# Optimization experiments

Hardware: AMD Instinct MI355X
Metric: run time of the kernel (lower is better)

The kernel has to match this reference:

```python
import jax, jax.numpy as jnp
import numpy as np

B, N, D, K, S = 16, 1024, 256, 16, 512
TEMP = 0.5   # self.temperature, set externally in the repo
EPS = 1e-10


def _gumbel(key, shape):
    u = jax.random.uniform(key, shape, dtype=jnp.float32)
    return -jnp.log(-jnp.log(u + EPS) + EPS)


def setup_inputs() -> dict:
    key = jax.random.key(0)
    k1, k2, k3 = jax.random.split(key, 3)
    return {
        "ze": jax.random.normal(k1, (B, N, D), dtype=jnp.float32),
        "c_logits": jax.random.normal(k2, (B, K), dtype=jnp.float32),
        "books": jax.random.normal(k3, (K, S, D), dtype=jnp.float32),
        "log_param_q": jnp.asarray(np.log(0.5), dtype=jnp.float32),
        "log_param_q_cls": jnp.asarray(np.log(0.5), dtype=jnp.float32),
        "is_train": 1,
    }


def reference(ze, c_logits, books, log_param_q, log_param_q_cls, is_train):
    # training-path forward of GaussianVectorQuantizer
    param_q = 1.0 + jnp.exp(log_param_q)
    precision_q = 0.5 / jnp.clip(param_q, 1e-10)
    param_q_cls = 1.0 + jnp.exp(log_param_q_cls)
    precision_q_cls = 0.5 / jnp.clip(param_q_cls, 1e-10)

    gkey = jax.random.key(42)
    kg1, kg2 = jax.random.split(gkey)

    # gumbel-softmax over clusters: (B, K)
    c_probs = jax.nn.softmax(
        (c_logits * precision_q_cls + _gumbel(kg1, c_logits.shape)) / TEMP, axis=-1
    )

    # pairwise squared distances to every codebook entry of every cluster: (B, N, K, S)
    z2 = jnp.sum(ze * ze, axis=-1)[:, :, None, None]          # (B, N, 1, 1)
    b2 = jnp.sum(books * books, axis=-1)[None, None]          # (1, 1, K, S)
    cross = jnp.einsum('bnd,ksd->bnks', ze, books)            # (B, N, K, S)
    logit_all = -(z2 - 2.0 * cross + b2) * precision_q        # (B, N, K, S)

    # cluster-probability-weighted logits: (B, N, S)
    logits = jnp.einsum('bnks,bk->bns', logit_all, c_probs)

    # gumbel-softmax encodings per cluster, then weighted codebook matmul
    enc = jax.nn.softmax((logit_all + _gumbel(kg2, logit_all.shape)) / TEMP, axis=-1)
    zq = jnp.einsum('bnks,ksd,bk->bnd', enc, books, c_probs)  # (B, N, D)

    prob = jax.nn.softmax(logits, axis=-1)
    log_prob = jax.nn.log_softmax(logits, axis=-1)
    return zq, precision_q, prob, log_prob
```

## Files before the change

### kernel.cpp

```cpp
#include <hip/hip_runtime.h>
#include <cstdint>
#include <cstddef>

#define JAX_PARTITIONABLE 1

namespace {

constexpr int Bsz = 16, Nn = 1024, Dd = 256, Kk = 16, Ss = 512;
constexpr uint32_t BN = (uint32_t)Bsz * Nn;
constexpr int ZQ_SIZE = Bsz * Nn * Dd;
constexpr int PQ_OFF = ZQ_SIZE;
constexpr int PROB_OFF = ZQ_SIZE + 1;
constexpr int BNS = Bsz * Nn * Ss;
constexpr int LP_OFF = PROB_OFF + BNS;

constexpr int WS_CP = 0;
constexpr int WS_B2 = 256;
constexpr int WS_WB2 = WS_B2 + Kk * Ss;
constexpr int WS_WBOOKS = WS_WB2 + Bsz * Ss;
constexpr int WS_BBF = WS_WBOOKS + Bsz * Ss * Dd;
constexpr int WS_BTF = WS_BBF + (Kk * Ss * Dd) / 2;

typedef __attribute__((ext_vector_type(8))) short bf16x8;
typedef __attribute__((ext_vector_type(4))) short short4v;
typedef __attribute__((ext_vector_type(4))) float f32x4;

struct KP { uint32_t a, b; };

__host__ __device__ constexpr KP tf2x32(uint32_t k0, uint32_t k1,
                                        uint32_t x0, uint32_t x1) {
  uint32_t ks[3] = {k0, k1, k0 ^ k1 ^ 0x1BD11BDAu};
  const int rot[2][4] = {{13, 15, 26, 6}, {17, 29, 16, 24}};
  x0 += ks[0];
  x1 += ks[1];
#pragma unroll
  for (int i = 0; i < 5; ++i) {
#pragma unroll
    for (int j = 0; j < 4; ++j) {
      int r = rot[i & 1][j];
      x0 += x1;
      x1 = (x1 << r) | (x1 >> (32 - r));
      x1 ^= x0;
    }
    x0 += ks[(i + 1) % 3];
    x1 += ks[(i + 2) % 3] + (uint32_t)(i + 1);
  }
  return {x0, x1};
}

#if JAX_PARTITIONABLE
constexpr KP KG1 = tf2x32(0u, 42u, 0u, 0u);
constexpr KP KG2 = tf2x32(0u, 42u, 0u, 1u);
#else
constexpr KP KH0 = tf2x32(0u, 42u, 0u, 2u);
constexpr KP KH1 = tf2x32(0u, 42u, 1u, 3u);
constexpr KP KG1 = {KH0.a, KH1.a};
constexpr KP KG2 = {KH0.b, KH1.b};
#endif

__device__ __forceinline__ float jax_gumbel(KP key, uint32_t idx, uint32_t half) {
#if JAX_PARTITIONABLE
  (void)half;
  KP h = tf2x32(key.a, key.b, 0u, idx);
  uint32_t bits = h.a ^ h.b;
#else
  uint32_t lo = idx < half ? idx : idx - half;
  KP h = tf2x32(key.a, key.b, lo, lo + half);
  uint32_t bits = idx < half ? h.a : h.b;
#endif
  float u = __uint_as_float((bits >> 9) | 0x3F800000u) - 1.0f;
  return -__logf(-__logf(u + 1e-10f) + 1e-10f);
}

__device__ __forceinline__ float prec_q(const float* p) {
  return 0.5f / fmaxf(1.0f + expf(p[0]), 1e-10f);
}

__device__ __forceinline__ short f2bf(float x) {
  uint32_t u = __float_as_uint(x);
  uint32_t r = (u + 0x7FFFu + ((u >> 16) & 1u)) >> 16;
  return (short)r;
}

__global__ void __launch_bounds__(256) cprobs_kernel(
    const float* __restrict__ c_logits, const float* __restrict__ lpq,
    const float* __restrict__ lpq_cls, float* __restrict__ ws,
    float* __restrict__ out) {
  __shared__ float sl[256];
  const int t = threadIdx.x;
  const float pqc = prec_q(lpq_cls);
  float g = jax_gumbel(KG1, (uint32_t)t, 128u);
  sl[t] = (c_logits[t] * pqc + g) * 2.0f;
  __syncthreads();
  const int b = t >> 4;
  float m = -3.0e38f;
  for (int j = 0; j < 16; ++j) m = fmaxf(m, sl[b * 16 + j]);
  float sum = 0.f;
  for (int j = 0; j < 16; ++j) sum += expf(sl[b * 16 + j] - m);
  ws[WS_CP + t] = expf(sl[t] - m) / sum;
  if (t == 0) out[PQ_OFF] = prec_q(lpq);
}

__global__ void __launch_bounds__(256) norms_kernel(
    const float* __restrict__ books, float* __restrict__ ws) {
  const int row = blockIdx.x * 4 + (threadIdx.x >> 6);
  const int lane = threadIdx.x & 63;
  float4 v = ((const float4*)(books + (size_t)row * Dd))[lane];
  float s = v.x * v.x + v.y * v.y + v.z * v.z + v.w * v.w;
#pragma unroll
  for (int d = 1; d < 64; d <<= 1) s += __shfl_xor(s, d);
  if (lane == 0) ws[WS_B2 + row] = s;
}

__global__ void __launch_bounds__(256) prep_kernel(
    const float* __restrict__ books, float* __restrict__ ws) {
  __shared__ short tile[16 * 256];
  const int k = blockIdx.x >> 5;
  const int s0 = (blockIdx.x & 31) << 4;
  short* bbf = (short*)(ws + WS_BBF);
  short* btf = (short*)(ws + WS_BTF);
  const int t = threadIdx.x;
#pragma unroll
  for (int i = 0; i < 4; ++i) {
    int idx = t + 256 * i;
    int r = idx >> 6, dq = idx & 63;
    float4 v = ((const float4*)books)[(size_t)(k * Ss + s0 + r) * 64 + dq];
    short4v h = {f2bf(v.x), f2bf(v.y), f2bf(v.z), f2bf(v.w)};
    *(short4v*)&bbf[(size_t)(k * Ss + s0 + r) * 256 + dq * 4] = h;
    *(short4v*)&tile[r * 256 + dq * 4] = h;
  }
  __syncthreads();
  const int d = t;
  short vals[16];
#pragma unroll
  for (int r = 0; r < 16; ++r) vals[r] = tile[r * 256 + d];
  bf16x8 lo, hi;
#pragma unroll
  for (int r = 0; r < 8; ++r) { lo[r] = vals[r]; hi[r] = vals[r + 8]; }
  size_t base = ((size_t)(k * 256 + d)) * 512 + s0;
  *(bf16x8*)&btf[base] = lo;
  *(bf16x8*)&btf[base + 8] = hi;
}

__global__ void __launch_bounds__(256) wbooks_kernel(
    const float* __restrict__ books, float* __restrict__ ws) {
  const int bs = blockIdx.x;
  const int b = bs >> 9, s = bs & 511;
  const int d = threadIdx.x;
  const float* cp = ws + WS_CP + b * 16;
  float acc = 0.f;
#pragma unroll
  for (int k = 0; k < 16; ++k)
    acc = fmaf(cp[k], books[((size_t)(k * Ss + s)) * Dd + d], acc);
  ws[WS_WBOOKS + ((size_t)(b * Ss + s)) * Dd + d] = acc;
  if (d == 0) {
    float a2 = 0.f;
#pragma unroll
    for (int k = 0; k < 16; ++k) a2 = fmaf(cp[k], ws[WS_B2 + k * Ss + s], a2);
    ws[WS_WB2 + b * Ss + s] = a2;
  }
}

__global__ void __launch_bounds__(256, 4) logits_kernel(
    const float* __restrict__ ze, const float* __restrict__ lpq,
    const float* __restrict__ ws, float* __restrict__ out) {
  __shared__ float ze_s[8 * 256];
  __shared__ float ls[8 * 512];
  const int b = blockIdx.x >> 7;
  const int n0 = (blockIdx.x & 127) << 3;
  const int t = threadIdx.x;
  const float pq = prec_q(lpq);

  {
    const float4* zin = (const float4*)(ze + (size_t)(b * Nn + n0) * Dd);
    float4* zo = (float4*)ze_s;
    zo[t] = zin[t];
    zo[t + 256] = zin[t + 256];
  }
  __syncthreads();

  float acc0[8], acc1[8];
#pragma unroll
  for (int r = 0; r < 8; ++r) { acc0[r] = 0.f; acc1[r] = 0.f; }
  const int s0 = t, s1 = t + 256;
  const float4* w4_0 = (const float4*)(ws + WS_WBOOKS + (size_t)(b * Ss + s0) * Dd);
  const float4* w4_1 = (const float4*)(ws + WS_WBOOKS + (size_t)(b * Ss + s1) * Dd);
  const float4* z4 = (const float4*)ze_s;
  for (int dq = 0; dq < 64; ++dq) {
    float4 u0 = w4_0[dq], u1 = w4_1[dq];
#pragma unroll
    for (int r = 0; r < 8; ++r) {
      float4 z = z4[r * 64 + dq];
      acc0[r] = fmaf(z.x, u0.x, fmaf(z.y, u0.y, fmaf(z.z, u0.z, fmaf(z.w, u0.w, acc0[r]))));
      acc1[r] = fmaf(z.x, u1.x, fmaf(z.y, u1.y, fmaf(z.z, u1.z, fmaf(z.w, u1.w, acc1[r]))));
    }
  }
  const float wb2v0 = ws[WS_WB2 + b * Ss + s0];
  const float wb2v1 = ws[WS_WB2 + b * Ss + s1];
#pragma unroll
  for (int r = 0; r < 8; ++r) {
    ls[r * 512 + s0] = pq * (2.f * acc0[r] - wb2v0);
    ls[r * 512 + s1] = pq * (2.f * acc1[r] - wb2v1);
  }
  __syncthreads();

  const int r = t >> 5, c = t & 31;
  float m = -3.0e38f;
#pragma unroll
  for (int j = 0; j < 16; ++j) m = fmaxf(m, ls[r * 512 + c + 32 * j]);
#pragma unroll
  for (int d = 1; d < 32; d <<= 1) m = fmaxf(m, __shfl_xor(m, d));
  float ev[16];
  float sum = 0.f;
#pragma unroll
  for (int j = 0; j < 16; ++j) {
    ev[j] = expf(ls[r * 512 + c + 32 * j] - m);
    sum += ev[j];
  }
#pragma unroll
  for (int d = 1; d < 32; d <<= 1) sum += __shfl_xor(sum, d);
  const float inv = 1.f / sum;
  const float lsum = logf(sum);
  const size_t obase = (size_t)(b * Nn + n0 + r) * Ss;
  float* pr = out + PROB_OFF + obase;
  float* lp = out + LP_OFF + obase;
#pragma unroll
  for (int j = 0; j < 16; ++j) {
    int s = c + 32 * j;
    pr[s] = ev[j] * inv;
    lp[s] = (ls[r * 512 + s] - m) - lsum;
  }
}

__global__ void __launch_bounds__(512, 4) zq_kernel(
    const float* __restrict__ ze, const float* __restrict__ lpq,
    const float* __restrict__ ws, float* __restrict__ out) {
  __shared__ short ze_s[32 * 264];
  __shared__ short enc_s[32 * 520];
  __shared__ float redmax[8][32];
  __shared__ float redsum[8][32];
  __shared__ float finalM[32];
  __shared__ float finalT[32];
  __shared__ float cpk[16];

  const int b = blockIdx.x >> 5;
  const int n0 = (blockIdx.x & 31) << 5;
  const int t = threadIdx.x;
  const int w = t >> 6, lane = t & 63, c = lane & 15, q = lane >> 4;
  const float pq = prec_q(lpq);
  const short* bbf = (const short*)(ws + WS_BBF);
  const short* btf = (const short*)(ws + WS_BTF);
  const float* b2p = ws + WS_B2;

  if (t < 16) cpk[t] = ws[WS_CP + b * 16 + t];
#pragma unroll
  for (int i = 0; i < 4; ++i) {
    int idx = t + 512 * i;
    int r = idx >> 6, dq = idx & 63;
    float4 v = ((const float4*)ze)[(size_t)(b * Nn + n0 + r) * 64 + dq];
    short4v h = {f2bf(v.x), f2bf(v.y), f2bf(v.z), f2bf(v.w)};
    *(short4v*)&ze_s[r * 264 + dq * 4] = h;
  }
  __syncthreads();

  f32x4 acc2[2][2];
#pragma unroll
  for (int rt = 0; rt < 2; ++rt)
#pragma unroll
    for (int dt = 0; dt < 2; ++dt) acc2[rt][dt] = (f32x4)(0.f);

  for (int k = 0; k < 16; ++k) {
    f32x4 acc1[2][4];
#pragma unroll
    for (int rt = 0; rt < 2; ++rt)
#pragma unroll
      for (int st = 0; st < 4; ++st) acc1[rt][st] = (f32x4)(0.f);
    for (int dstep = 0; dstep < 8; ++dstep) {
      bf16x8 a0 = *(const bf16x8*)&ze_s[(c) * 264 + dstep * 32 + q * 8];
      bf16x8 a1 = *(const bf16x8*)&ze_s[(16 + c) * 264 + dstep * 32 + q * 8];
#pragma unroll
      for (int st = 0; st < 4; ++st) {
        bf16x8 bB = *(const bf16x8*)&bbf[((size_t)(k * Ss + w * 64 + st * 16 + c)) * 256 +
                                         dstep * 32 + q * 8];
        acc1[0][st] = __builtin_amdgcn_mfma_f32_16x16x32_bf16(a0, bB, acc1[0][st], 0, 0, 0);
        acc1[1][st] = __builtin_amdgcn_mfma_f32_16x16x32_bf16(a1, bB, acc1[1][st], 0, 0, 0);
      }
    }

    float b2v[4];
#pragma unroll
    for (int st = 0; st < 4; ++st) b2v[st] = b2p[k * Ss + w * 64 + st * 16 + c];
    float mx[2][4], sm[2][4];
#pragma unroll
    for (int rt = 0; rt < 2; ++rt)
#pragma unroll
      for (int reg = 0; reg < 4; ++reg) mx[rt][reg] = -3.0e38f;
#pragma unroll
    for (int rt = 0; rt < 2; ++rt)
#pragma unroll
      for (int st = 0; st < 4; ++st)
#pragma unroll
        for (int reg = 0; reg < 4; ++reg) {
          int row = n0 + rt * 16 + q * 4 + reg;
          uint32_t gi = ((uint32_t)(b * Nn + row) * (uint32_t)Kk + (uint32_t)k) * (uint32_t)Ss +
                        (uint32_t)(w * 64 + st * 16 + c);
          float g = jax_gumbel(KG2, gi, 0u);
          float v = ((2.f * acc1[rt][st][reg] - b2v[st]) * pq + g) * 2.f;
          acc1[rt][st][reg] = v;
          mx[rt][reg] = fmaxf(mx[rt][reg], v);
        }
#pragma unroll
    for (int m = 1; m < 16; m <<= 1)
#pragma unroll
      for (int rt = 0; rt < 2; ++rt)
#pragma unroll
        for (int reg = 0; reg < 4; ++reg)
          mx[rt][reg] = fmaxf(mx[rt][reg], __shfl_xor(mx[rt][reg], m));
#pragma unroll
    for (int rt = 0; rt < 2; ++rt)
#pragma unroll
      for (int reg = 0; reg < 4; ++reg) sm[rt][reg] = 0.f;
#pragma unroll
    for (int rt = 0; rt < 2; ++rt)
#pragma unroll
      for (int st = 0; st < 4; ++st)
#pragma unroll
        for (int reg = 0; reg < 4; ++reg) {
          float e = __expf(acc1[rt][st][reg] - mx[rt][reg]);
          acc1[rt][st][reg] = e;
          sm[rt][reg] += e;
        }
#pragma unroll
    for (int m = 1; m < 16; m <<= 1)
#pragma unroll
      for (int rt = 0; rt < 2; ++rt)
#pragma unroll
        for (int reg = 0; reg < 4; ++reg) sm[rt][reg] += __shfl_xor(sm[rt][reg], m);
    if (c == 0) {
#pragma unroll
      for (int rt = 0; rt < 2; ++rt)
#pragma unroll
        for (int reg = 0; reg < 4; ++reg) {
          int rl = rt * 16 + q * 4 + reg;
          redmax[w][rl] = mx[rt][reg];
          redsum[w][rl] = sm[rt][reg];
        }
    }
    __syncthreads();
    if (t < 32) {
      float M = redmax[0][t];
#pragma unroll
      for (int w2 = 1; w2 < 8; ++w2) M = fmaxf(M, redmax[w2][t]);
      float T = 0.f;
#pragma unroll
      for (int w2 = 0; w2 < 8; ++w2) T += redsum[w2][t] * __expf(redmax[w2][t] - M);
      finalM[t] = M;
      finalT[t] = 1.f / T;
    }
    __syncthreads();

    const float cpv = cpk[k];
#pragma unroll
    for (int rt = 0; rt < 2; ++rt)
#pragma unroll
      for (int reg = 0; reg < 4; ++reg) {
        int rl = rt * 16 + q * 4 + reg;
        float scale = cpv * __expf(mx[rt][reg] - finalM[rl]) * finalT[rl];
#pragma unroll
        for (int st = 0; st < 4; ++st)
          enc_s[rl * 520 + w * 64 + st * 16 + c] = f2bf(acc1[rt][st][reg] * scale);
      }
    __syncthreads();

    for (int ss = 0; ss < 16; ++ss) {
      bf16x8 a0 = *(const bf16x8*)&enc_s[(c) * 520 + ss * 32 + q * 8];
      bf16x8 a1 = *(const bf16x8*)&enc_s[(16 + c) * 520 + ss * 32 + q * 8];
#pragma unroll
      for (int dt = 0; dt < 2; ++dt) {
        bf16x8 bB = *(const bf16x8*)&btf[((size_t)(k * 256 + w * 32 + dt * 16 + c)) * 512 +
                                         ss * 32 + q * 8];
        acc2[0][dt] = __builtin_amdgcn_mfma_f32_16x16x32_bf16(a0, bB, acc2[0][dt], 0, 0, 0);
        acc2[1][dt] = __builtin_amdgcn_mfma_f32_16x16x32_bf16(a1, bB, acc2[1][dt], 0, 0, 0);
      }
    }
    __syncthreads();
  }

#pragma unroll
  for (int rt = 0; rt < 2; ++rt)
#pragma unroll
    for (int dt = 0; dt < 2; ++dt)
#pragma unroll
      for (int reg = 0; reg < 4; ++reg) {
        int row = n0 + rt * 16 + q * 4 + reg;
        int d = w * 32 + dt * 16 + c;
        out[(size_t)(b * Nn + row) * Dd + d] = acc2[rt][dt][reg];
      }
}

}

extern "C" void kernel_launch(void* const* d_in, const int* in_sizes, int n_in,
                              void* d_out, int out_size, void* d_ws, size_t ws_size,
                              hipStream_t stream) {
  (void)in_sizes; (void)n_in; (void)out_size; (void)ws_size;
  const float* ze = (const float*)d_in[0];
  const float* c_logits = (const float*)d_in[1];
  const float* books = (const float*)d_in[2];
  const float* lpq = (const float*)d_in[3];
  const float* lpq_cls = (const float*)d_in[4];
  float* out = (float*)d_out;
  float* ws = (float*)d_ws;

  hipLaunchKernelGGL(cprobs_kernel, dim3(1), dim3(256), 0, stream,
                     c_logits, lpq, lpq_cls, ws, out);
  hipLaunchKernelGGL(norms_kernel, dim3(Kk * Ss / 4), dim3(256), 0, stream, books, ws);
  hipLaunchKernelGGL(prep_kernel, dim3(Kk * 32), dim3(256), 0, stream, books, ws);
  hipLaunchKernelGGL(wbooks_kernel, dim3(Bsz * Ss), dim3(256), 0, stream, books, ws);
  hipLaunchKernelGGL(logits_kernel, dim3(Bsz * (Nn / 8)), dim3(256), 0, stream,
                     ze, lpq, ws, out);
  hipLaunchKernelGGL(zq_kernel, dim3(Bsz * (Nn / 32)), dim3(512), 0, stream,
                     ze, lpq, ws, out);
}
```

Before: 885.0 us.

## Shrink zq_kernel row tile to 16 with 256-thread blocks and fewer barriers

New measurement: 1.216 ms. 1.37x slower.

```diff
diff --git a/kernel.cpp b/kernel.cpp
--- a/kernel.cpp
+++ b/kernel.cpp
@@ -232,19 +232,17 @@
   }
 }
 
-__global__ void __launch_bounds__(512, 4) zq_kernel(
+__global__ void __launch_bounds__(256, 4) zq_kernel(
     const float* __restrict__ ze, const float* __restrict__ lpq,
     const float* __restrict__ ws, float* __restrict__ out) {
-  __shared__ short ze_s[32 * 264];
-  __shared__ short enc_s[32 * 520];
-  __shared__ float redmax[8][32];
-  __shared__ float redsum[8][32];
-  __shared__ float finalM[32];
-  __shared__ float finalT[32];
+  __shared__ short ze_s[16 * 264];
+  __shared__ short enc_s[16 * 520];
+  __shared__ float redmax[4][16];
+  __shared__ float redsum[4][16];
   __shared__ float cpk[16];
 
-  const int b = blockIdx.x >> 5;
-  const int n0 = (blockIdx.x & 31) << 5;
+  const int b = blockIdx.x >> 6;
+  const int n0 = (blockIdx.x & 63) << 4;
   const int t = threadIdx.x;
   const int w = t >> 6, lane = t & 63, c = lane & 15, q = lane >> 4;
   const float pq = prec_q(lpq);
@@ -255,7 +253,7 @@
   if (t < 16) cpk[t] = ws[WS_CP + b * 16 + t];
 #pragma unroll
   for (int i = 0; i < 4; ++i) {
-    int idx = t + 512 * i;
+    int idx = t + 256 * i;
     int r = idx >> 6, dq = idx & 63;
     float4 v = ((const float4*)ze)[(size_t)(b * Nn + n0 + r) * 64 + dq];
     short4v h = {f2bf(v.x), f2bf(v.y), f2bf(v.z), f2bf(v.w)};
@@ -263,139 +261,110 @@
   }
   __syncthreads();
 
-  f32x4 acc2[2][2];
-#pragma unroll
-  for (int rt = 0; rt < 2; ++rt)
-#pragma unroll
-    for (int dt = 0; dt < 2; ++dt) acc2[rt][dt] = (f32x4)(0.f);
+  f32x4 acc2[4];
+#pragma unroll
+  for (int dt = 0; dt < 4; ++dt) acc2[dt] = (f32x4)(0.f);
+
+  const uint32_t rowbase = (uint32_t)(b * Nn + n0 + q * 4);
 
   for (int k = 0; k < 16; ++k) {
-    f32x4 acc1[2][4];
-#pragma unroll
-    for (int rt = 0; rt < 2; ++rt)
-#pragma unroll
-      for (int st = 0; st < 4; ++st) acc1[rt][st] = (f32x4)(0.f);
+    f32x4 acc1[8];
+#pragma unroll
+    for (int st = 0; st < 8; ++st) acc1[st] = (f32x4)(0.f);
     for (int dstep = 0; dstep < 8; ++dstep) {
-      bf16x8 a0 = *(const bf16x8*)&ze_s[(c) * 264 + dstep * 32 + q * 8];
-      bf16x8 a1 = *(const bf16x8*)&ze_s[(16 + c) * 264 + dstep * 32 + q * 8];
-#pragma unroll
-      for (int st = 0; st < 4; ++st) {
-        bf16x8 bB = *(const bf16x8*)&bbf[((size_t)(k * Ss + w * 64 + st * 16 + c)) * 256 +
+      bf16x8 a0 = *(const bf16x8*)&ze_s[c * 264 + dstep * 32 + q * 8];
+#pragma unroll
+      for (int st = 0; st < 8; ++st) {
+        bf16x8 bB = *(const bf16x8*)&bbf[((size_t)(k * Ss + w * 128 + st * 16 + c)) * 256 +
                                          dstep * 32 + q * 8];
-        acc1[0][st] = __builtin_amdgcn_mfma_f32_16x16x32_bf16(a0, bB, acc1[0][st], 0, 0, 0);
-        acc1[1][st] = __builtin_amdgcn_mfma_f32_16x16x32_bf16(a1, bB, acc1[1][st], 0, 0, 0);
-      }
-    }
-
-    float b2v[4];
-#pragma unroll
-    for (int st = 0; st < 4; ++st) b2v[st] = b2p[k * Ss + w * 64 + st * 16 + c];
-    float mx[2][4], sm[2][4];
-#pragma unroll
-    for (int rt = 0; rt < 2; ++rt)
-#pragma unroll
-      for (int reg = 0; reg < 4; ++reg) mx[rt][reg] = -3.0e38f;
-#pragma unroll
-    for (int rt = 0; rt < 2; ++rt)
-#pragma unroll
-      for (int st = 0; st < 4; ++st)
-#pragma unroll
-        for (int reg = 0; reg < 4; ++reg) {
-          int row = n0 + rt * 16 + q * 4 + reg;
-          uint32_t gi = ((uint32_t)(b * Nn + row) * (uint32_t)Kk + (uint32_t)k) * (uint32_t)Ss +
-                        (uint32_t)(w * 64 + st * 16 + c);
-          float g = jax_gumbel(KG2, gi, 0u);
-          float v = ((2.f * acc1[rt][st][reg] - b2v[st]) * pq + g) * 2.f;
-          acc1[rt][st][reg] = v;
-          mx[rt][reg] = fmaxf(mx[rt][reg], v);
-        }
+        acc1[st] = __builtin_amdgcn_mfma_f32_16x16x32_bf16(a0, bB, acc1[st], 0, 0, 0);
+      }
+    }
+
+    float b2v[8];
+#pragma unroll
+    for (int st = 0; st < 8; ++st) b2v[st] = b2p[k * Ss + w * 128 + st * 16 + c];
+    float mx[4], sm[4];
+#pragma unroll
+    for (int reg = 0; reg < 4; ++reg) mx[reg] = -3.0e38f;
+#pragma unroll
+    for (int st = 0; st < 8; ++st)
+#pragma unroll
+      for (int reg = 0; reg < 4; ++reg) {
+        uint32_t gi = ((rowbase + reg) * (uint32_t)Kk + (uint32_t)k) * (uint32_t)Ss +
+                      (uint32_t)(w * 128 + st * 16 + c);
+        float g = jax_gumbel(KG2, gi, 0u);
+        float v = ((2.f * acc1[st][reg] - b2v[st]) * pq + g) * 2.f;
+        acc1[st][reg] = v;
+        mx[reg] = fmaxf(mx[reg], v);
+      }
 #pragma unroll
     for (int m = 1; m < 16; m <<= 1)
 #pragma unroll
-      for (int rt = 0; rt < 2; ++rt)
-#pragma unroll
-        for (int reg = 0; reg < 4; ++reg)
-          mx[rt][reg] = fmaxf(mx[rt][reg], __shfl_xor(mx[rt][reg], m));
-#pragma unroll
-    for (int rt = 0; rt < 2; ++rt)
-#pragma unroll
-      for (int reg = 0; reg < 4; ++reg) sm[rt][reg] = 0.f;
-#pragma unroll
-    for (int rt = 0; rt < 2; ++rt)
-#pragma unroll
-      for (int st = 0; st < 4; ++st)
-#pragma unroll
-        for (int reg = 0; reg < 4; ++reg) {
-          float e = __expf(acc1[rt][st][reg] - mx[rt][reg]);
-          acc1[rt][st][reg] = e;
-          sm[rt][reg] += e;
-        }
+      for (int reg = 0; reg < 4; ++reg)
+        mx[reg] = fmaxf(mx[reg], __shfl_xor(mx[reg], m));
+#pragma unroll
+    for (int reg = 0; reg < 4; ++reg) sm[reg] = 0.f;
+#pragma unroll
+    for (int st = 0; st < 8; ++st)
+#pragma unroll
+      for (int reg = 0; reg < 4; ++reg) {
+        float e = __expf(acc1[st][reg] - mx[reg]);
+        acc1[st][reg] = e;
+        sm[reg] += e;
+      }
 #pragma unroll
     for (int m = 1; m < 16; m <<= 1)
 #pragma unroll
-      for (int rt = 0; rt < 2; ++rt)
-#pragma unroll
-        for (int reg = 0; reg < 4; ++reg) sm[rt][reg] += __shfl_xor(sm[rt][reg], m);
+      for (int reg = 0; reg < 4; ++reg) sm[reg] += __shfl_xor(sm[reg], m);
     if (c == 0) {
 #pragma unroll
-      for (int rt = 0; rt < 2; ++rt)
-#pragma unroll
-        for (int reg = 0; reg < 4; ++reg) {
-          int rl = rt * 16 + q * 4 + reg;
-          redmax[w][rl] = mx[rt][reg];
-          redsum[w][rl] = sm[rt][reg];
-        }
+      for (int reg = 0; reg < 4; ++reg) {
+        redmax[w][q * 4 + reg] = mx[reg];
+        redsum[w][q * 4 + reg] = sm[reg];
+      }
     }
     __syncthreads();
-    if (t < 32) {
-      float M = redmax[0][t];
-#pragma unroll
-      for (int w2 = 1; w2 < 8; ++w2) M = fmaxf(M, redmax[w2][t]);
+
+    const float cpv = cpk[k];
+    float scale[4];
+#pragma unroll
+    for (int reg = 0; reg < 4; ++reg) {
+      int rl = q * 4 + reg;
+      float M = redmax[0][rl];
+#pragma unroll
+      for (int w2 = 1; w2 < 4; ++w2) M = fmaxf(M, redmax[w2][rl]);
       float T = 0.f;
 #pragma unroll
-      for (int w2 = 0; w2 < 8; ++w2) T += redsum[w2][t] * __expf(redmax[w2][t] - M);
-      finalM[t] = M;
-      finalT[t] = 1.f / T;
-    }
+      for (int w2 = 0; w2 < 4; ++w2) T += redsum[w2][rl] * __expf(redmax[w2][rl] - M);
+      scale[reg] = cpv * __expf(mx[reg] - M) / T;
+    }
+#pragma unroll
+    for (int st = 0; st < 8; ++st)
+#pragma unroll
+      for (int reg = 0; reg < 4; ++reg)
+        enc_s[(q * 4 + reg) * 520 + w * 128 + st * 16 + c] = f2bf(acc1[st][reg] * scale[reg]);
     __syncthreads();
 
-    const float cpv = cpk[k];
-#pragma unroll
-    for (int rt = 0; rt < 2; ++rt)
-#pragma unroll
-      for (int reg = 0; reg < 4; ++reg) {
-        int rl = rt * 16 + q * 4 + reg;
-        float scale = cpv * __expf(mx[rt][reg] - finalM[rl]) * finalT[rl];
-#pragma unroll
-        for (int st = 0; st < 4; ++st)
-          enc_s[rl * 520 + w * 64 + st * 16 + c] = f2bf(acc1[rt][st][reg] * scale);
-      }
-    __syncthreads();
-
     for (int ss = 0; ss < 16; ++ss) {
-      bf16x8 a0 = *(const bf16x8*)&enc_s[(c) * 520 + ss * 32 + q * 8];
-      bf16x8 a1 = *(const bf16x8*)&enc_s[(16 + c) * 520 + ss * 32 + q * 8];
-#pragma unroll
-      for (int dt = 0; dt < 2; ++dt) {
-        bf16x8 bB = *(const bf16x8*)&btf[((size_t)(k * 256 + w * 32 + dt * 16 + c)) * 512 +
+      bf16x8 aE = *(const bf16x8*)&enc_s[c * 520 + ss * 32 + q * 8];
+#pragma unroll
+      for (int dt = 0; dt < 4; ++dt) {
+        bf16x8 bB = *(const bf16x8*)&btf[((size_t)(k * 256 + w * 64 + dt * 16 + c)) * 512 +
                                          ss * 32 + q * 8];
-        acc2[0][dt] = __builtin_amdgcn_mfma_f32_16x16x32_bf16(a0, bB, acc2[0][dt], 0, 0, 0);
-        acc2[1][dt] = __builtin_amdgcn_mfma_f32_16x16x32_bf16(a1, bB, acc2[1][dt], 0, 0, 0);
-      }
-    }
-    __syncthreads();
-  }
-
-#pragma unroll
-  for (int rt = 0; rt < 2; ++rt)
-#pragma unroll
-    for (int dt = 0; dt < 2; ++dt)
-#pragma unroll
-      for (int reg = 0; reg < 4; ++reg) {
-        int row = n0 + rt * 16 + q * 4 + reg;
-        int d = w * 32 + dt * 16 + c;
-        out[(size_t)(b * Nn + row) * Dd + d] = acc2[rt][dt][reg];
-      }
+        acc2[dt] = __builtin_amdgcn_mfma_f32_16x16x32_bf16(aE, bB, acc2[dt], 0, 0, 0);
+      }
+    }
+  }
+
+#pragma unroll
+  for (int dt = 0; dt < 4; ++dt)
+#pragma unroll
+    for (int reg = 0; reg < 4; ++reg) {
+      int row = n0 + q * 4 + reg;
+      int d = w * 64 + dt * 16 + c;
+      out[(size_t)(b * Nn + row) * Dd + d] = acc2[dt][reg];
+    }
 }
 
 }
@@ -419,6 +388,6 @@
   hipLaunchKernelGGL(wbooks_kernel, dim3(Bsz * Ss), dim3(256), 0, stream, books, ws);
   hipLaunchKernelGGL(logits_kernel, dim3(Bsz * (Nn / 8)), dim3(256), 0, stream,
                      ze, lpq, ws, out);
-  hipLaunchKernelGGL(zq_kernel, dim3(Bsz * (Nn / 32)), dim3(512), 0, stream,
+  hipLaunchKernelGGL(zq_kernel, dim3(Bsz * (Nn / 16)), dim3(256), 0, stream,
                      ze, lpq, ws, out);
 }
```
